# Optimization experiments

Hardware: AMD Instinct MI355X
Metric: run time of the kernel (lower is better)

Reference implementation:

```python
import jax, jax.numpy as jnp
import numpy as np

HEADS = 8
DIM_HEAD = 64
SCALE = DIM_HEAD ** -0.5
EPS = 1e-5


def layernorm(t, g, b):
    mu = t.mean(-1, keepdims=True)
    var = ((t - mu) ** 2).mean(-1, keepdims=True)
    return (t - mu) * jax.lax.rsqrt(var + EPS) * g + b


def setup_inputs() -> dict:
    key = jax.random.key(0)
    ks = jax.random.split(key, 12)
    b, n, dim, inner = 2, 2048, 512, HEADS * DIM_HEAD
    s = dim ** -0.5
    return {
        "x": jax.random.normal(ks[0], (b, n, dim), jnp.float32),
        "context": jax.random.normal(ks[1], (b, n, dim), jnp.float32),
        "g_x": jnp.ones((dim,), jnp.float32),
        "b_x": jnp.zeros((dim,), jnp.float32),
        "g_c": jnp.ones((dim,), jnp.float32),
        "b_c": jnp.zeros((dim,), jnp.float32),
        "W_qk": jax.random.normal(ks[2], (dim, inner), jnp.float32) * s,
        "W_cqk": jax.random.normal(ks[3], (dim, inner), jnp.float32) * s,
        "W_v": jax.random.normal(ks[4], (dim, inner), jnp.float32) * s,
        "W_cv": jax.random.normal(ks[5], (dim, inner), jnp.float32) * s,
        "W_out": jax.random.normal(ks[6], (inner, dim), jnp.float32) * s,
        "b_out": jnp.zeros((dim,), jnp.float32),
        "W_cout": jax.random.normal(ks[7], (inner, dim), jnp.float32) * s,
        "b_cout": jnp.zeros((dim,), jnp.float32),
    }


def reference(x, context, g_x, b_x, g_c, b_c, W_qk, W_cqk, W_v, W_cv, W_out, b_out, W_cout, b_cout):
    b, i, _ = x.shape
    j = context.shape[1]
    xn = layernorm(x, g_x, b_x)
    cn = layernorm(context, g_c, b_c)

    def split_heads(t):  # [b, n, h*d] -> [b, h, n, d]
        return t.reshape(t.shape[0], t.shape[1], HEADS, DIM_HEAD).transpose(0, 2, 1, 3)

    qk = split_heads(xn @ W_qk)
    cqk = split_heads(cn @ W_cqk)
    v = split_heads(xn @ W_v)
    cv = split_heads(cn @ W_cv)

    sim = jnp.einsum('bhid,bhjd->bhij', qk, cqk) * SCALE  # [b,h,i,j]
    attn = jax.nn.softmax(sim, axis=-1)           # rows: x attends to context
    context_attn = jax.nn.softmax(sim, axis=-2)   # cols: context attends to x

    out = jnp.einsum('bhij,bhjd->bhid', attn, cv)            # [b,h,i,d]
    context_out = jnp.einsum('bhij,bhid->bhjd', context_attn, v)  # [b,h,j,d]

    def merge_heads(t):  # [b,h,n,d] -> [b,n,h*d]
        return t.transpose(0, 2, 1, 3).reshape(t.shape[0], t.shape[2], HEADS * DIM_HEAD)

    out = merge_heads(out) @ W_out + b_out
    context_out = merge_heads(context_out) @ W_cout + b_cout
    return out, context_out
```

## Files before the change

kernel.cpp:

```cpp
#include <hip/hip_runtime.h>


typedef _Float16 half_t;
typedef __attribute__((ext_vector_type(2))) _Float16 half2v;
typedef __attribute__((ext_vector_type(4))) _Float16 half4v;
typedef __attribute__((ext_vector_type(8))) _Float16 half8v;
typedef __attribute__((ext_vector_type(4))) float floatx4;

#define MFMA16(a, b, c) __builtin_amdgcn_mfma_f32_16x16x32_f16((a), (b), (c), 0, 0, 0)

#if defined(__has_builtin)
#if __has_builtin(__builtin_amdgcn_exp2f)
#define EXP2F(x) __builtin_amdgcn_exp2f(x)
#else
#define EXP2F(x) exp2f(x)
#endif
#else
#define EXP2F(x) exp2f(x)
#endif

__device__ __forceinline__ half2v pk2(float a, float b) {
#if defined(__has_builtin) && __has_builtin(__builtin_amdgcn_cvt_pkrtz)
    union { __fp16 __attribute__((ext_vector_type(2))) i; half2v o; } u;
    u.i = __builtin_amdgcn_cvt_pkrtz(a, b);
    return u.o;
#else
    half2v r; r[0] = (half_t)a; r[1] = (half_t)b; return r;
#endif
}

__device__ __forceinline__ void gld16(const half_t* g, half_t* l) {
    __builtin_amdgcn_global_load_lds(
        (const __attribute__((address_space(1))) void*)g,
        (__attribute__((address_space(3))) void*)l, 16, 0, 0);
}

__global__ __launch_bounds__(256) void prep_kernel(
    const float* __restrict__ x, const float* __restrict__ ctx,
    const float* __restrict__ gx, const float* __restrict__ bx,
    const float* __restrict__ gc, const float* __restrict__ bc,
    half_t* __restrict__ xn, half_t* __restrict__ cn,
    const float* __restrict__ W0, const float* __restrict__ W1,
    const float* __restrict__ W2, const float* __restrict__ W3,
    const float* __restrict__ W4, const float* __restrict__ W5,
    half_t* __restrict__ Wt)
{
    __shared__ alignas(16) half_t Ts[128][136];
    const int blk = blockIdx.x;
    const int tid = threadIdx.x;
    const int wave = tid >> 6, lane = tid & 63;

    if (blk < 2048) {
        const int row = blk * 4 + wave;
        const float *src, *g, *b;
        half_t* dst;
        if (row < 4096) {
            src = x + (size_t)row * 512; g = gx; b = bx; dst = xn + (size_t)row * 512;
        } else {
            const size_t r = (size_t)(row - 4096);
            src = ctx + r * 512; g = gc; b = bc; dst = cn + r * 512;
        }
        const float4 a0 = *(const float4*)(src + lane * 4);
        const float4 a1 = *(const float4*)(src + 256 + lane * 4);
        float s = a0.x + a0.y + a0.z + a0.w + a1.x + a1.y + a1.z + a1.w;
        float q = a0.x * a0.x + a0.y * a0.y + a0.z * a0.z + a0.w * a0.w +
                  a1.x * a1.x + a1.y * a1.y + a1.z * a1.z + a1.w * a1.w;
#pragma unroll
        for (int m = 1; m < 64; m <<= 1) {
            s += __shfl_xor(s, m);
            q += __shfl_xor(q, m);
        }
        const float mean = s * (1.0f / 512.0f);
        const float var = q * (1.0f / 512.0f) - mean * mean;
        const float rs = rsqrtf(var + 1e-5f);
        const float4 g0 = *(const float4*)(g + lane * 4);
        const float4 g1 = *(const float4*)(g + 256 + lane * 4);
        const float4 b0 = *(const float4*)(b + lane * 4);
        const float4 b1 = *(const float4*)(b + 256 + lane * 4);
        half4v h0, h1;
        h0[0] = (half_t)((a0.x - mean) * rs * g0.x + b0.x);
        h0[1] = (half_t)((a0.y - mean) * rs * g0.y + b0.y);
        h0[2] = (half_t)((a0.z - mean) * rs * g0.z + b0.z);
        h0[3] = (half_t)((a0.w - mean) * rs * g0.w + b0.w);
        h1[0] = (half_t)((a1.x - mean) * rs * g1.x + b1.x);
        h1[1] = (half_t)((a1.y - mean) * rs * g1.y + b1.y);
        h1[2] = (half_t)((a1.z - mean) * rs * g1.z + b1.z);
        h1[3] = (half_t)((a1.w - mean) * rs * g1.w + b1.w);
        *(half4v*)(dst + lane * 4) = h0;
        *(half4v*)(dst + 256 + lane * 4) = h1;
        return;
    }

    const int b2 = blk - 2048;
    const int mat = b2 >> 4, tile = b2 & 15;
    const float* src;
    switch (mat) {
        case 0: src = W0; break;
        case 1: src = W1; break;
        case 2: src = W2; break;
        case 3: src = W3; break;
        case 4: src = W4; break;
        default: src = W5; break;
    }
    const int tr0 = (tile >> 2) * 128;
    const int tc0 = (tile & 3) * 128;
#pragma unroll
    for (int p = 0; p < 16; ++p) {
        const int idx = p * 256 + tid;
        const int r = idx >> 5, c4 = (idx & 31) * 4;
        const float4 w = *(const float4*)(src + (size_t)(tr0 + r) * 512 + tc0 + c4);
        Ts[c4 + 0][r] = (half_t)w.x;
        Ts[c4 + 1][r] = (half_t)w.y;
        Ts[c4 + 2][r] = (half_t)w.z;
        Ts[c4 + 3][r] = (half_t)w.w;
    }
    __syncthreads();
    half_t* dst = Wt + (size_t)mat * 262144;
#pragma unroll
    for (int p = 0; p < 8; ++p) {
        const int idx = p * 256 + tid;
        const int row = idx >> 4, ch = (idx & 15) * 8;
        *(half8v*)(dst + (size_t)(tc0 + row) * 512 + tr0 + ch) = *(const half8v*)&Ts[row][ch];
    }
}

__global__ __launch_bounds__(256) void gemm_in_kernel(
    const half_t* __restrict__ xn, const half_t* __restrict__ cn,
    const half_t* __restrict__ Wt,
    half_t* __restrict__ qk, half_t* __restrict__ v_t,
    half_t* __restrict__ cqk, half_t* __restrict__ cv_t)
{
    const half_t* A; const half_t* B; half_t* O;
    switch (blockIdx.z) {
        case 0:  A = xn; B = Wt;          O = qk;   break;
        case 1:  A = xn; B = Wt + 262144; O = v_t;  break;
        case 2:  A = cn; B = Wt + 524288; O = cqk;  break;
        default: A = cn; B = Wt + 786432; O = cv_t; break;
    }
    const int tr = blockIdx.z & 1;
    const int mt0 = blockIdx.x * 128;
    const int nt0 = blockIdx.y * 128;

    __shared__ alignas(16) half_t As[128 * 64];
    __shared__ alignas(16) half_t Ws[128 * 64];

    const int tid = threadIdx.x;
    const int wave = tid >> 6, lane = tid & 63;
    const int wr = wave >> 1, wc = wave & 1;
    const int q4 = lane >> 4, c = lane & 15;

    int srow[4], scol[4];
#pragma unroll
    for (int p = 0; p < 4; ++p) {
        const int ofs = p * 4096 + wave * 1024 + lane * 16;
        const int row = ofs >> 7;
        const int pc = (ofs >> 4) & 7;
        srow[p] = row;
        scol[p] = (pc ^ (row & 7)) * 8;
    }

    const half_t* P1 = tr ? As : Ws;
    const half_t* P2 = tr ? Ws : As;

    const floatx4 z4 = {0.f, 0.f, 0.f, 0.f};
    floatx4 acc[4][4];
#pragma unroll
    for (int mt = 0; mt < 4; ++mt)
#pragma unroll
        for (int nt = 0; nt < 4; ++nt) acc[mt][nt] = z4;

    for (int kb = 0; kb < 8; ++kb) {
        const int k0 = kb * 64;
#pragma unroll
        for (int p = 0; p < 4; ++p) {
            const int lofs = p * 2048 + wave * 512;
            gld16(A + (size_t)(mt0 + srow[p]) * 512 + k0 + scol[p], As + lofs);
            gld16(B + (size_t)(nt0 + srow[p]) * 512 + k0 + scol[p], Ws + lofs);
        }
        __syncthreads();
#pragma unroll
        for (int kt = 0; kt < 2; ++kt) {
            half8v f1[4], f2[4];
#pragma unroll
            for (int i = 0; i < 4; ++i) {
                const int r1 = wr * 64 + i * 16 + c;
                const int r2 = wc * 64 + i * 16 + c;
                f1[i] = *(const half8v*)&P1[(r1 << 6) + (((kt * 4 + q4) ^ (r1 & 7)) << 3)];
                f2[i] = *(const half8v*)&P2[(r2 << 6) + (((kt * 4 + q4) ^ (r2 & 7)) << 3)];
            }
#pragma unroll
            for (int mt = 0; mt < 4; ++mt)
#pragma unroll
                for (int nt = 0; nt < 4; ++nt)
                    acc[mt][nt] = MFMA16(f1[mt], f2[nt], acc[mt][nt]);
        }
        __syncthreads();
    }

    const int bb = mt0 >> 11;
    const int nnb = mt0 & 2047;
    if (tr) {
#pragma unroll
        for (int mt = 0; mt < 4; ++mt) {
            const int row = nnb + wr * 64 + mt * 16 + q4 * 4;
#pragma unroll
            for (int nt = 0; nt < 4; ++nt) {
                const int col = nt0 + wc * 64 + nt * 16 + c;
                const int h = col >> 6, dd = col & 63;
                half4v pk;
                pk[0] = (half_t)acc[mt][nt][0];
                pk[1] = (half_t)acc[mt][nt][1];
                pk[2] = (half_t)acc[mt][nt][2];
                pk[3] = (half_t)acc[mt][nt][3];
                *(half4v*)(O + ((size_t)(bb * 8 + h) * 64 + dd) * 2048 + row) = pk;
            }
        }
    } else {
#pragma unroll
        for (int mt = 0; mt < 4; ++mt) {
            const int colw = nt0 + wr * 64 + mt * 16 + q4 * 4;
            const int h = colw >> 6, dd = colw & 63;
#pragma unroll
            for (int nt = 0; nt < 4; ++nt) {
                const int row = nnb + wc * 64 + nt * 16 + c;
                half4v pk;
                pk[0] = (half_t)acc[mt][nt][0];
                pk[1] = (half_t)acc[mt][nt][1];
                pk[2] = (half_t)acc[mt][nt][2];
                pk[3] = (half_t)acc[mt][nt][3];
                *(half4v*)(O + ((size_t)(bb * 8 + h) * 2048 + row) * 64 + dd) = pk;
            }
        }
    }
}

__global__ __launch_bounds__(256, 2) void flash_kernel(
    const half_t* __restrict__ qk, const half_t* __restrict__ cqk,
    const half_t* __restrict__ v_t, const half_t* __restrict__ cv_t,
    half_t* __restrict__ out_h, half_t* __restrict__ ctx_out_h)
{
    const int bh = blockIdx.x, it = blockIdx.y, dir = blockIdx.z;
    const half_t* Q  = dir ? cqk : qk;
    const half_t* K  = dir ? qk  : cqk;
    const half_t* VT = dir ? v_t : cv_t;
    half_t* Out = dir ? ctx_out_h : out_h;
    const half_t* Qb = Q + (size_t)bh * (2048 * 64);
    const half_t* Kb = K + (size_t)bh * (2048 * 64);
    const half_t* VTb = VT + (size_t)bh * (64 * 2048);

    __shared__ alignas(16) half_t Ks[128 * 64];
    __shared__ alignas(16) half_t CVs[64 * 128];

    const int tid = threadIdx.x;
    const int wave = tid >> 6, lane = tid & 63;
    const int q4 = lane >> 4, c = lane & 15;

    half8v onesb;
#pragma unroll
    for (int j = 0; j < 8; ++j) onesb[j] = (c == 0) ? (half_t)1.0f : (half_t)0.0f;

    half8v qf[2][2];
#pragma unroll
    for (int mt = 0; mt < 2; ++mt)
#pragma unroll
        for (int kt = 0; kt < 2; ++kt) {
            half8v v = *(const half8v*)(Qb + (size_t)(it * 128 + wave * 32 + mt * 16 + c) * 64 +
                                        kt * 32 + q4 * 8);
            qf[mt][kt] = v * (half_t)0.18033688f;
        }

    const floatx4 z4 = {0.f, 0.f, 0.f, 0.f};
    floatx4 accT[4][2];
    floatx4 accL[2];
#pragma unroll
    for (int vt = 0; vt < 4; ++vt)
#pragma unroll
        for (int mt = 0; mt < 2; ++mt) accT[vt][mt] = z4;
    accL[0] = z4; accL[1] = z4;

    half8v kpre[4], vpre[4];
#pragma unroll
    for (int p = 0; p < 4; ++p) {
        const int cidx = p * 256 + tid;
        kpre[p] = *(const half8v*)(Kb + (size_t)(cidx >> 3) * 64 + (cidx & 7) * 8);
        vpre[p] = *(const half8v*)(VTb + (size_t)(cidx >> 4) * 2048 + (cidx & 15) * 8);
    }

    for (int jt = 0; jt < 16; ++jt) {
        __syncthreads();
#pragma unroll
        for (int p = 0; p < 4; ++p) {
            const int cidx = p * 256 + tid;
            const int krow = cidx >> 3, kch = cidx & 7;
            *(half8v*)&Ks[krow * 64 + ((kch ^ ((krow >> 2) & 7)) * 8)] = kpre[p];
            const int vrow = cidx >> 4, vch = cidx & 15;
            *(half8v*)&CVs[vrow * 128 + ((vch ^ (vrow & 15)) * 8)] = vpre[p];
        }
        __syncthreads();
        if (jt < 15) {
            const half_t* Kt = Kb + (size_t)(jt + 1) * 8192;
            const half_t* Vt = VTb + (jt + 1) * 128;
#pragma unroll
            for (int p = 0; p < 4; ++p) {
                const int cidx = p * 256 + tid;
                kpre[p] = *(const half8v*)(Kt + (size_t)(cidx >> 3) * 64 + (cidx & 7) * 8);
                vpre[p] = *(const half8v*)(Vt + (size_t)(cidx >> 4) * 2048 + (cidx & 15) * 8);
            }
        }

#pragma unroll
        for (int g = 0; g < 4; ++g) {
            floatx4 st[2][2];
#pragma unroll
            for (int t = 0; t < 2; ++t) {
                const int jr = g * 32 + t * 4 + ((c >> 2) << 3) + (c & 3);
                const int sw = (jr >> 2) & 7;
                const half8v kf0 = *(const half8v*)&Ks[jr * 64 + ((q4 ^ sw) * 8)];
                const half8v kf1 = *(const half8v*)&Ks[jr * 64 + (((4 + q4) ^ sw) * 8)];
#pragma unroll
                for (int mt = 0; mt < 2; ++mt) {
                    floatx4 tt = MFMA16(kf0, qf[mt][0], z4);
                    st[mt][t] = MFMA16(kf1, qf[mt][1], tt);
                }
            }
            half8v pf[2];
#pragma unroll
            for (int mt = 0; mt < 2; ++mt) {
                union { half8v v; half2v h2[4]; } u;
                u.h2[0] = pk2(EXP2F(fminf(st[mt][0][0], 15.0f)),
                              EXP2F(fminf(st[mt][0][1], 15.0f)));
                u.h2[1] = pk2(EXP2F(fminf(st[mt][0][2], 15.0f)),
                              EXP2F(fminf(st[mt][0][3], 15.0f)));
                u.h2[2] = pk2(EXP2F(fminf(st[mt][1][0], 15.0f)),
                              EXP2F(fminf(st[mt][1][1], 15.0f)));
                u.h2[3] = pk2(EXP2F(fminf(st[mt][1][2], 15.0f)),
                              EXP2F(fminf(st[mt][1][3], 15.0f)));
                pf[mt] = u.v;
            }
#pragma unroll
            for (int vt = 0; vt < 4; ++vt) {
                const half8v bf = *(const half8v*)&CVs[(vt * 16 + c) * 128 +
                                                       (((g * 4 + q4) ^ c) * 8)];
#pragma unroll
                for (int mt = 0; mt < 2; ++mt)
                    accT[vt][mt] = MFMA16(bf, pf[mt], accT[vt][mt]);
            }
#pragma unroll
            for (int mt = 0; mt < 2; ++mt)
                accL[mt] = MFMA16(onesb, pf[mt], accL[mt]);
        }
    }

    const size_t ob = (size_t)(bh >> 3) * 2048 * 512 + (size_t)(bh & 7) * 64;
#pragma unroll
    for (int mt = 0; mt < 2; ++mt) {
        const float l = __shfl(accL[mt][0], c);
        const float rl = 1.0f / l;
        const int row = it * 128 + wave * 32 + mt * 16 + c;
#pragma unroll
        for (int vt = 0; vt < 4; ++vt) {
            half4v pk;
            pk[0] = (half_t)(accT[vt][mt][0] * rl);
            pk[1] = (half_t)(accT[vt][mt][1] * rl);
            pk[2] = (half_t)(accT[vt][mt][2] * rl);
            pk[3] = (half_t)(accT[vt][mt][3] * rl);
            *(half4v*)(Out + ob + (size_t)row * 512 + vt * 16 + q4 * 4) = pk;
        }
    }
}

__global__ __launch_bounds__(256) void gemm_out_kernel(
    const half_t* __restrict__ out_h, const half_t* __restrict__ ctx_out_h,
    const half_t* __restrict__ Wt,
    const float* __restrict__ bout, const float* __restrict__ bcout,
    float* __restrict__ dout)
{
    const half_t* A; const half_t* B; const float* bias; float* O;
    if (blockIdx.z == 0) { A = out_h;     B = Wt + 1048576; bias = bout;  O = dout; }
    else                 { A = ctx_out_h; B = Wt + 1310720; bias = bcout; O = dout + 2097152; }

    const int mt0 = blockIdx.x * 64;
    const int nt0 = blockIdx.y * 128;

    __shared__ alignas(16) half_t As[64 * 64];
    __shared__ alignas(16) half_t Ws[128 * 64];

    const int tid = threadIdx.x;
    const int wave = tid >> 6, lane = tid & 63;
    const int wr = wave >> 1, wc = wave & 1;
    const int q4 = lane >> 4, c = lane & 15;

    int srow[4], scol[4];
#pragma unroll
    for (int p = 0; p < 4; ++p) {
        const int ofs = p * 4096 + wave * 1024 + lane * 16;
        const int row = ofs >> 7;
        const int pc = (ofs >> 4) & 7;
        srow[p] = row;
        scol[p] = (pc ^ (row & 7)) * 8;
    }

    const floatx4 z4 = {0.f, 0.f, 0.f, 0.f};
    floatx4 acc[4][2];
#pragma unroll
    for (int mt = 0; mt < 4; ++mt)
#pragma unroll
        for (int nt = 0; nt < 2; ++nt) acc[mt][nt] = z4;

    for (int kb = 0; kb < 8; ++kb) {
        const int k0 = kb * 64;
#pragma unroll
        for (int p = 0; p < 4; ++p) {
            const int lofs = p * 2048 + wave * 512;
            gld16(B + (size_t)(nt0 + srow[p]) * 512 + k0 + scol[p], Ws + lofs);
            if (p < 2)
                gld16(A + (size_t)(mt0 + srow[p]) * 512 + k0 + scol[p], As + lofs);
        }
        __syncthreads();
#pragma unroll
        for (int kt = 0; kt < 2; ++kt) {
            half8v f1[4], f2[2];
#pragma unroll
            for (int i = 0; i < 4; ++i) {
                const int r1 = wr * 64 + i * 16 + c;
                f1[i] = *(const half8v*)&Ws[(r1 << 6) + (((kt * 4 + q4) ^ (r1 & 7)) << 3)];
            }
#pragma unroll
            for (int i = 0; i < 2; ++i) {
                const int r2 = wc * 32 + i * 16 + c;
                f2[i] = *(const half8v*)&As[(r2 << 6) + (((kt * 4 + q4) ^ (r2 & 7)) << 3)];
            }
#pragma unroll
            for (int mt = 0; mt < 4; ++mt)
#pragma unroll
                for (int nt = 0; nt < 2; ++nt)
                    acc[mt][nt] = MFMA16(f1[mt], f2[nt], acc[mt][nt]);
        }
        __syncthreads();
    }

#pragma unroll
    for (int mt = 0; mt < 4; ++mt) {
        const int col = nt0 + wr * 64 + mt * 16 + q4 * 4;
        const float4 bv = *(const float4*)(bias + col);
#pragma unroll
        for (int nt = 0; nt < 2; ++nt) {
            const int row = mt0 + wc * 32 + nt * 16 + c;
            float4 o;
            o.x = acc[mt][nt][0] + bv.x;
            o.y = acc[mt][nt][1] + bv.y;
            o.z = acc[mt][nt][2] + bv.z;
            o.w = acc[mt][nt][3] + bv.w;
            *(float4*)(O + (size_t)row * 512 + col) = o;
        }
    }
}

extern "C" void kernel_launch(void* const* d_in, const int* in_sizes, int n_in,
                              void* d_out, int out_size, void* d_ws, size_t ws_size,
                              hipStream_t stream)
{
    (void)in_sizes; (void)n_in; (void)out_size; (void)ws_size;
    const float* x      = (const float*)d_in[0];
    const float* ctx    = (const float*)d_in[1];
    const float* g_x    = (const float*)d_in[2];
    const float* b_x    = (const float*)d_in[3];
    const float* g_c    = (const float*)d_in[4];
    const float* b_c    = (const float*)d_in[5];
    const float* W_qk   = (const float*)d_in[6];
    const float* W_cqk  = (const float*)d_in[7];
    const float* W_v    = (const float*)d_in[8];
    const float* W_cv   = (const float*)d_in[9];
    const float* W_out  = (const float*)d_in[10];
    const float* b_out  = (const float*)d_in[11];
    const float* W_cout = (const float*)d_in[12];
    const float* b_cout = (const float*)d_in[13];
    float* out = (float*)d_out;

    half_t* ws = (half_t*)d_ws;
    const size_t SEG = 2097152;
    half_t* xn        = ws;
    half_t* cn        = ws + 1 * SEG;
    half_t* qk        = ws + 2 * SEG;
    half_t* cqk       = ws + 3 * SEG;
    half_t* v_t       = ws + 4 * SEG;
    half_t* cv_t      = ws + 5 * SEG;
    half_t* Wt        = ws + 6 * SEG;
    half_t* out_h     = xn;
    half_t* ctx_out_h = cn;

    prep_kernel<<<2144, 256, 0, stream>>>(x, ctx, g_x, b_x, g_c, b_c, xn, cn,
                                          W_qk, W_v, W_cqk, W_cv, W_out, W_cout, Wt);
    gemm_in_kernel<<<dim3(32, 4, 4), 256, 0, stream>>>(xn, cn, Wt, qk, v_t, cqk, cv_t);
    flash_kernel<<<dim3(16, 16, 2), 256, 0, stream>>>(qk, cqk, v_t, cv_t, out_h, ctx_out_h);
    gemm_out_kernel<<<dim3(64, 4, 2), 256, 0, stream>>>(out_h, ctx_out_h, Wt, b_out, b_cout, out);
}
```

Measured before the change: 175.1 us.

## Split flash kernel rows across 8 waves with 16 rows each

The flash kernel moves from 256 to 512 threads per block, so each wave owns 16 query rows instead of 32. That halves the per-wave accumulators and Q fragments, and the K/V tile load loop is spread over twice as many threads. The K shared-memory swizzle also changes to XOR in the low row bits, aiming to cut LDS bank conflicts. The trade-off is that each K/V fragment read from LDS now feeds half as many MFMAs, and block-level synchronization covers more waves.

```diff
diff --git a/kernel.cpp b/kernel.cpp
--- a/kernel.cpp
+++ b/kernel.cpp
@@ -234,7 +234,7 @@
     }
 }
 
-__global__ __launch_bounds__(256, 2) void flash_kernel(
+__global__ __launch_bounds__(512, 4) void flash_kernel(
     const half_t* __restrict__ qk, const half_t* __restrict__ cqk,
     const half_t* __restrict__ v_t, const half_t* __restrict__ cv_t,
     half_t* __restrict__ out_h, half_t* __restrict__ ctx_out_h)
@@ -259,29 +259,25 @@
 #pragma unroll
     for (int j = 0; j < 8; ++j) onesb[j] = (c == 0) ? (half_t)1.0f : (half_t)0.0f;
 
-    half8v qf[2][2];
-#pragma unroll
-    for (int mt = 0; mt < 2; ++mt)
-#pragma unroll
-        for (int kt = 0; kt < 2; ++kt) {
-            half8v v = *(const half8v*)(Qb + (size_t)(it * 128 + wave * 32 + mt * 16 + c) * 64 +
-                                        kt * 32 + q4 * 8);
-            qf[mt][kt] = v * (half_t)0.18033688f;
-        }
+    half8v qf[2];
+#pragma unroll
+    for (int kt = 0; kt < 2; ++kt) {
+        half8v v = *(const half8v*)(Qb + (size_t)(it * 128 + wave * 16 + c) * 64 +
+                                    kt * 32 + q4 * 8);
+        qf[kt] = v * (half_t)0.18033688f;
+    }
 
     const floatx4 z4 = {0.f, 0.f, 0.f, 0.f};
-    floatx4 accT[4][2];
-    floatx4 accL[2];
-#pragma unroll
-    for (int vt = 0; vt < 4; ++vt)
-#pragma unroll
-        for (int mt = 0; mt < 2; ++mt) accT[vt][mt] = z4;
-    accL[0] = z4; accL[1] = z4;
-
-    half8v kpre[4], vpre[4];
-#pragma unroll
-    for (int p = 0; p < 4; ++p) {
-        const int cidx = p * 256 + tid;
+    floatx4 accT[4];
+    floatx4 accL;
+#pragma unroll
+    for (int vt = 0; vt < 4; ++vt) accT[vt] = z4;
+    accL = z4;
+
+    half8v kpre[2], vpre[2];
+#pragma unroll
+    for (int p = 0; p < 2; ++p) {
+        const int cidx = p * 512 + tid;
         kpre[p] = *(const half8v*)(Kb + (size_t)(cidx >> 3) * 64 + (cidx & 7) * 8);
         vpre[p] = *(const half8v*)(VTb + (size_t)(cidx >> 4) * 2048 + (cidx & 15) * 8);
     }
@@ -289,10 +285,11 @@
     for (int jt = 0; jt < 16; ++jt) {
         __syncthreads();
 #pragma unroll
-        for (int p = 0; p < 4; ++p) {
-            const int cidx = p * 256 + tid;
+        for (int p = 0; p < 2; ++p) {
+            const int cidx = p * 512 + tid;
             const int krow = cidx >> 3, kch = cidx & 7;
-            *(half8v*)&Ks[krow * 64 + ((kch ^ ((krow >> 2) & 7)) * 8)] = kpre[p];
+            const int ksw = ((krow >> 2) ^ (krow & 3)) & 7;
+            *(half8v*)&Ks[krow * 64 + ((kch ^ ksw) * 8)] = kpre[p];
             const int vrow = cidx >> 4, vch = cidx & 15;
             *(half8v*)&CVs[vrow * 128 + ((vch ^ (vrow & 15)) * 8)] = vpre[p];
         }
@@ -301,8 +298,8 @@
             const half_t* Kt = Kb + (size_t)(jt + 1) * 8192;
             const half_t* Vt = VTb + (jt + 1) * 128;
 #pragma unroll
-            for (int p = 0; p < 4; ++p) {
-                const int cidx = p * 256 + tid;
+            for (int p = 0; p < 2; ++p) {
+                const int cidx = p * 512 + tid;
                 kpre[p] = *(const half8v*)(Kt + (size_t)(cidx >> 3) * 64 + (cidx & 7) * 8);
                 vpre[p] = *(const half8v*)(Vt + (size_t)(cidx >> 4) * 2048 + (cidx & 15) * 8);
             }
@@ -310,62 +307,51 @@
 
 #pragma unroll
         for (int g = 0; g < 4; ++g) {
-            floatx4 st[2][2];
+            floatx4 st[2];
 #pragma unroll
             for (int t = 0; t < 2; ++t) {
                 const int jr = g * 32 + t * 4 + ((c >> 2) << 3) + (c & 3);
-                const int sw = (jr >> 2) & 7;
+                const int sw = ((jr >> 2) ^ (jr & 3)) & 7;
                 const half8v kf0 = *(const half8v*)&Ks[jr * 64 + ((q4 ^ sw) * 8)];
                 const half8v kf1 = *(const half8v*)&Ks[jr * 64 + (((4 + q4) ^ sw) * 8)];
-#pragma unroll
-                for (int mt = 0; mt < 2; ++mt) {
-                    floatx4 tt = MFMA16(kf0, qf[mt][0], z4);
-                    st[mt][t] = MFMA16(kf1, qf[mt][1], tt);
-                }
-            }
-            half8v pf[2];
-#pragma unroll
-            for (int mt = 0; mt < 2; ++mt) {
+                floatx4 tt = MFMA16(kf0, qf[0], z4);
+                st[t] = MFMA16(kf1, qf[1], tt);
+            }
+            half8v pf;
+            {
                 union { half8v v; half2v h2[4]; } u;
-                u.h2[0] = pk2(EXP2F(fminf(st[mt][0][0], 15.0f)),
-                              EXP2F(fminf(st[mt][0][1], 15.0f)));
-                u.h2[1] = pk2(EXP2F(fminf(st[mt][0][2], 15.0f)),
-                              EXP2F(fminf(st[mt][0][3], 15.0f)));
-                u.h2[2] = pk2(EXP2F(fminf(st[mt][1][0], 15.0f)),
-                              EXP2F(fminf(st[mt][1][1], 15.0f)));
-                u.h2[3] = pk2(EXP2F(fminf(st[mt][1][2], 15.0f)),
-                              EXP2F(fminf(st[mt][1][3], 15.0f)));
-                pf[mt] = u.v;
+                u.h2[0] = pk2(EXP2F(fminf(st[0][0], 15.0f)),
+                              EXP2F(fminf(st[0][1], 15.0f)));
+                u.h2[1] = pk2(EXP2F(fminf(st[0][2], 15.0f)),
+                              EXP2F(fminf(st[0][3], 15.0f)));
+                u.h2[2] = pk2(EXP2F(fminf(st[1][0], 15.0f)),
+                              EXP2F(fminf(st[1][1], 15.0f)));
+                u.h2[3] = pk2(EXP2F(fminf(st[1][2], 15.0f)),
+                              EXP2F(fminf(st[1][3], 15.0f)));
+                pf = u.v;
             }
 #pragma unroll
             for (int vt = 0; vt < 4; ++vt) {
                 const half8v bf = *(const half8v*)&CVs[(vt * 16 + c) * 128 +
                                                        (((g * 4 + q4) ^ c) * 8)];
-#pragma unroll
-                for (int mt = 0; mt < 2; ++mt)
-                    accT[vt][mt] = MFMA16(bf, pf[mt], accT[vt][mt]);
-            }
-#pragma unroll
-            for (int mt = 0; mt < 2; ++mt)
-                accL[mt] = MFMA16(onesb, pf[mt], accL[mt]);
+                accT[vt] = MFMA16(bf, pf, accT[vt]);
+            }
+            accL = MFMA16(onesb, pf, accL);
         }
     }
 
     const size_t ob = (size_t)(bh >> 3) * 2048 * 512 + (size_t)(bh & 7) * 64;
-#pragma unroll
-    for (int mt = 0; mt < 2; ++mt) {
-        const float l = __shfl(accL[mt][0], c);
-        const float rl = 1.0f / l;
-        const int row = it * 128 + wave * 32 + mt * 16 + c;
-#pragma unroll
-        for (int vt = 0; vt < 4; ++vt) {
-            half4v pk;
-            pk[0] = (half_t)(accT[vt][mt][0] * rl);
-            pk[1] = (half_t)(accT[vt][mt][1] * rl);
-            pk[2] = (half_t)(accT[vt][mt][2] * rl);
-            pk[3] = (half_t)(accT[vt][mt][3] * rl);
-            *(half4v*)(Out + ob + (size_t)row * 512 + vt * 16 + q4 * 4) = pk;
-        }
+    const float l = __shfl(accL[0], c);
+    const float rl = 1.0f / l;
+    const int row = it * 128 + wave * 16 + c;
+#pragma unroll
+    for (int vt = 0; vt < 4; ++vt) {
+        half4v pk;
+        pk[0] = (half_t)(accT[vt][0] * rl);
+        pk[1] = (half_t)(accT[vt][1] * rl);
+        pk[2] = (half_t)(accT[vt][2] * rl);
+        pk[3] = (half_t)(accT[vt][3] * rl);
+        *(half4v*)(Out + ob + (size_t)row * 512 + vt * 16 + q4 * 4) = pk;
     }
 }
 
@@ -492,6 +478,6 @@
     prep_kernel<<<2144, 256, 0, stream>>>(x, ctx, g_x, b_x, g_c, b_c, xn, cn,
                                           W_qk, W_v, W_cqk, W_cv, W_out, W_cout, Wt);
     gemm_in_kernel<<<dim3(32, 4, 4), 256, 0, stream>>>(xn, cn, Wt, qk, v_t, cqk, cv_t);
-    flash_kernel<<<dim3(16, 16, 2), 256, 0, stream>>>(qk, cqk, v_t, cv_t, out_h, ctx_out_h);
+    flash_kernel<<<dim3(16, 16, 2), 512, 0, stream>>>(qk, cqk, v_t, cv_t, out_h, ctx_out_h);
     gemm_out_kernel<<<dim3(64, 4, 2), 256, 0, stream>>>(out_h, ctx_out_h, Wt, b_out, b_cout, out);
 }
```

New measurement: 171.7 us. Within noise of the previous version (-2.0%).

## Split flash attention over key halves with fp32 partials and a combine kernel

Applied to the files above, without the earlier changes.

The flash kernel now splits the key/context dimension into two halves, doubling the grid to 1024 blocks. Each block writes unnormalised fp32 partial outputs and row sums to a workspace, and a new combine kernel adds the halves, normalises, and writes the fp16 head-merged output. The change also raises the launch-bounds occupancy hint to 4 and alters the K shared-memory swizzle to reduce bank conflicts. The cost is an extra kernel launch and extra global traffic for the fp32 partials (about 32 MB written and read).

```diff
diff --git a/kernel.cpp b/kernel.cpp
--- a/kernel.cpp
+++ b/kernel.cpp
@@ -234,19 +234,21 @@
     }
 }
 
-__global__ __launch_bounds__(256, 2) void flash_kernel(
+__global__ __launch_bounds__(256, 4) void flash_kernel(
     const half_t* __restrict__ qk, const half_t* __restrict__ cqk,
     const half_t* __restrict__ v_t, const half_t* __restrict__ cv_t,
-    half_t* __restrict__ out_h, half_t* __restrict__ ctx_out_h)
+    float* __restrict__ Pbuf, float* __restrict__ Lbuf)
 {
-    const int bh = blockIdx.x, it = blockIdx.y, dir = blockIdx.z;
+    const int bh = blockIdx.x, it = blockIdx.y;
+    const int dir = blockIdx.z >> 1, js = blockIdx.z & 1;
     const half_t* Q  = dir ? cqk : qk;
     const half_t* K  = dir ? qk  : cqk;
     const half_t* VT = dir ? v_t : cv_t;
-    half_t* Out = dir ? ctx_out_h : out_h;
     const half_t* Qb = Q + (size_t)bh * (2048 * 64);
     const half_t* Kb = K + (size_t)bh * (2048 * 64);
     const half_t* VTb = VT + (size_t)bh * (64 * 2048);
+    float* Pb = Pbuf + (size_t)((js * 2 + dir) * 16 + bh) * (2048 * 64);
+    float* Lb = Lbuf + (size_t)((js * 2 + dir) * 16 + bh) * 2048;
 
     __shared__ alignas(16) half_t Ks[128 * 64];
     __shared__ alignas(16) half_t CVs[64 * 128];
@@ -278,26 +280,32 @@
         for (int mt = 0; mt < 2; ++mt) accT[vt][mt] = z4;
     accL[0] = z4; accL[1] = z4;
 
+    const int jt0 = js * 8;
     half8v kpre[4], vpre[4];
-#pragma unroll
-    for (int p = 0; p < 4; ++p) {
-        const int cidx = p * 256 + tid;
-        kpre[p] = *(const half8v*)(Kb + (size_t)(cidx >> 3) * 64 + (cidx & 7) * 8);
-        vpre[p] = *(const half8v*)(VTb + (size_t)(cidx >> 4) * 2048 + (cidx & 15) * 8);
-    }
-
-    for (int jt = 0; jt < 16; ++jt) {
+    {
+        const half_t* Kt = Kb + (size_t)jt0 * 8192;
+        const half_t* Vt = VTb + jt0 * 128;
+#pragma unroll
+        for (int p = 0; p < 4; ++p) {
+            const int cidx = p * 256 + tid;
+            kpre[p] = *(const half8v*)(Kt + (size_t)(cidx >> 3) * 64 + (cidx & 7) * 8);
+            vpre[p] = *(const half8v*)(Vt + (size_t)(cidx >> 4) * 2048 + (cidx & 15) * 8);
+        }
+    }
+
+    for (int jt = jt0; jt < jt0 + 8; ++jt) {
         __syncthreads();
 #pragma unroll
         for (int p = 0; p < 4; ++p) {
             const int cidx = p * 256 + tid;
             const int krow = cidx >> 3, kch = cidx & 7;
-            *(half8v*)&Ks[krow * 64 + ((kch ^ ((krow >> 2) & 7)) * 8)] = kpre[p];
+            const int ksw = ((krow >> 2) ^ (krow & 3)) & 7;
+            *(half8v*)&Ks[krow * 64 + ((kch ^ ksw) * 8)] = kpre[p];
             const int vrow = cidx >> 4, vch = cidx & 15;
             *(half8v*)&CVs[vrow * 128 + ((vch ^ (vrow & 15)) * 8)] = vpre[p];
         }
         __syncthreads();
-        if (jt < 15) {
+        if (jt < jt0 + 7) {
             const half_t* Kt = Kb + (size_t)(jt + 1) * 8192;
             const half_t* Vt = VTb + (jt + 1) * 128;
 #pragma unroll
@@ -314,7 +322,7 @@
 #pragma unroll
             for (int t = 0; t < 2; ++t) {
                 const int jr = g * 32 + t * 4 + ((c >> 2) << 3) + (c & 3);
-                const int sw = (jr >> 2) & 7;
+                const int sw = ((jr >> 2) ^ (jr & 3)) & 7;
                 const half8v kf0 = *(const half8v*)&Ks[jr * 64 + ((q4 ^ sw) * 8)];
                 const half8v kf1 = *(const half8v*)&Ks[jr * 64 + (((4 + q4) ^ sw) * 8)];
 #pragma unroll
@@ -351,22 +359,49 @@
         }
     }
 
-    const size_t ob = (size_t)(bh >> 3) * 2048 * 512 + (size_t)(bh & 7) * 64;
 #pragma unroll
     for (int mt = 0; mt < 2; ++mt) {
-        const float l = __shfl(accL[mt][0], c);
-        const float rl = 1.0f / l;
         const int row = it * 128 + wave * 32 + mt * 16 + c;
+        if (q4 == 0) Lb[row] = accL[mt][0];
 #pragma unroll
         for (int vt = 0; vt < 4; ++vt) {
-            half4v pk;
-            pk[0] = (half_t)(accT[vt][mt][0] * rl);
-            pk[1] = (half_t)(accT[vt][mt][1] * rl);
-            pk[2] = (half_t)(accT[vt][mt][2] * rl);
-            pk[3] = (half_t)(accT[vt][mt][3] * rl);
-            *(half4v*)(Out + ob + (size_t)row * 512 + vt * 16 + q4 * 4) = pk;
-        }
-    }
+            float4 o;
+            o.x = accT[vt][mt][0];
+            o.y = accT[vt][mt][1];
+            o.z = accT[vt][mt][2];
+            o.w = accT[vt][mt][3];
+            *(float4*)(Pb + (size_t)row * 64 + vt * 16 + q4 * 4) = o;
+        }
+    }
+}
+
+__global__ __launch_bounds__(256) void combine_kernel(
+    const float* __restrict__ Pbuf, const float* __restrict__ Lbuf,
+    half_t* __restrict__ out_h, half_t* __restrict__ ctx_out_h)
+{
+    const int tid = threadIdx.x;
+    const int rg = blockIdx.x * 16 + (tid >> 4);
+    const int q = tid & 15;
+    const int i = rg & 2047;
+    const int bh = (rg >> 11) & 15;
+    const int dir = rg >> 15;
+
+    const size_t pb0 = (size_t)(dir * 16 + bh) * (2048 * 64) + (size_t)i * 64 + q * 4;
+    const size_t pb1 = pb0 + (size_t)2 * 16 * 2048 * 64;
+    const float4 a0 = *(const float4*)(Pbuf + pb0);
+    const float4 a1 = *(const float4*)(Pbuf + pb1);
+    const size_t lb0 = (size_t)(dir * 16 + bh) * 2048 + i;
+    const float l = Lbuf[lb0] + Lbuf[lb0 + (size_t)2 * 16 * 2048];
+    const float rl = 1.0f / l;
+
+    half_t* Out = dir ? ctx_out_h : out_h;
+    half4v pk;
+    pk[0] = (half_t)((a0.x + a1.x) * rl);
+    pk[1] = (half_t)((a0.y + a1.y) * rl);
+    pk[2] = (half_t)((a0.z + a1.z) * rl);
+    pk[3] = (half_t)((a0.w + a1.w) * rl);
+    *(half4v*)(Out + (size_t)(bh >> 3) * 2048 * 512 + (size_t)i * 512 +
+               (bh & 7) * 64 + q * 4) = pk;
 }
 
 __global__ __launch_bounds__(256) void gemm_out_kernel(
@@ -488,10 +523,13 @@
     half_t* Wt        = ws + 6 * SEG;
     half_t* out_h     = xn;
     half_t* ctx_out_h = cn;
+    float* Pbuf = (float*)(ws + 6 * SEG + 1572864);
+    float* Lbuf = Pbuf + (size_t)2 * 2 * 16 * 2048 * 64;
 
     prep_kernel<<<2144, 256, 0, stream>>>(x, ctx, g_x, b_x, g_c, b_c, xn, cn,
                                           W_qk, W_v, W_cqk, W_cv, W_out, W_cout, Wt);
     gemm_in_kernel<<<dim3(32, 4, 4), 256, 0, stream>>>(xn, cn, Wt, qk, v_t, cqk, cv_t);
-    flash_kernel<<<dim3(16, 16, 2), 256, 0, stream>>>(qk, cqk, v_t, cv_t, out_h, ctx_out_h);
+    flash_kernel<<<dim3(16, 16, 4), 256, 0, stream>>>(qk, cqk, v_t, cv_t, Pbuf, Lbuf);
+    combine_kernel<<<4096, 256, 0, stream>>>(Pbuf, Lbuf, out_h, ctx_out_h);
     gemm_out_kernel<<<dim3(64, 4, 2), 256, 0, stream>>>(out_h, ctx_out_h, Wt, b_out, b_cout, out);
 }
```

After: 231.2 us. +32.1%, slower.
